# Kernel tuning notes

Hardware: AMD Instinct MI355X
Metric: run time of the kernel (lower is better)

Reference implementation:

```python
import jax, jax.numpy as jnp
import numpy as np

N, E, D = 100000, 1600000, 128
EPS = 1e-5
NUM_LAYERS = 5


def setup_inputs() -> dict:
    key = jax.random.key(0)
    ks = jax.random.split(key, 2 + 2 * NUM_LAYERS)
    inp = {
        "x": jax.random.normal(ks[0], (N, D), dtype=jnp.float32),
        "edge_index": jax.random.randint(ks[1], (2, E), 0, N),
    }
    for i in range(NUM_LAYERS):
        inp[f"W{i}"] = jax.random.normal(ks[2 + 2 * i], (D, D), dtype=jnp.float32) / np.sqrt(D).astype(np.float32)
        inp[f"b{i}"] = jax.random.normal(ks[3 + 2 * i], (D,), dtype=jnp.float32) * 0.01
    return inp


def _gcn_forward(x, edge_index, Ws, bs):
    src, dst = edge_index[0], edge_index[1]
    # Degree with self-loops (torch code appends arange(N) loops, then clamps
    # count at min=1; with loops deg >= 1 always, so clamp is a no-op).
    deg = jax.ops.segment_sum(jnp.ones((E,), x.dtype), dst, num_segments=N) + 1.0
    inv_deg = (1.0 / deg)[:, None]  # [N, 1]
    for W, b in zip(Ws, bs):
        h = x @ W.T  # [N, D] linear (no bias; bias added after aggregation)
        # mean aggregation over in-neighbors + self-loop message (= h itself)
        agg = (jax.ops.segment_sum(h[src], dst, num_segments=N) + h) * inv_deg + b
        # batch_norm in training mode, no affine, biased variance, eps=1e-5
        mean = agg.mean(axis=0)
        var = ((agg - mean) ** 2).mean(axis=0)
        x = jax.nn.relu((agg - mean) * jax.lax.rsqrt(var + EPS))
        # dropout p=0.0, eval mode -> identity
    return x


def reference(x, edge_index, W0, b0, W1, b1, W2, b2, W3, b3, W4, b4):
    return _gcn_forward(x, edge_index, (W0, W1, W2, W3, W4), (b0, b1, b2, b3, b4))
```

## Files before the change

### kernel.cpp

```cpp
#include <hip/hip_runtime.h>
#include <hip/hip_bf16.h>

#define DD 128
#define NPART 8

typedef __bf16 bf16x8 __attribute__((ext_vector_type(8)));
typedef float f32x4 __attribute__((ext_vector_type(4)));

__device__ inline unsigned short f2bf_rne(float f) {
    unsigned u = __float_as_uint(f);
    u += 0x7fff + ((u >> 16) & 1);
    return (unsigned short)(u >> 16);
}


__global__ __launch_bounds__(256) void hist_kernel(const int* __restrict__ dst,
                                                   int* __restrict__ cnt, int E, int psize) {
    int part = blockIdx.x & (NPART - 1);
    int lo = part * psize, hi = lo + psize;
    int stride = (gridDim.x >> 3) * 256;
    for (int e = (blockIdx.x >> 3) * 256 + threadIdx.x; e < E; e += stride) {
        int d = dst[e];
        if (d >= lo && d < hi) atomicAdd(&cnt[d], 1);
    }
}

__global__ void scanA_kernel(const int* __restrict__ cnt, int* __restrict__ row_off,
                             int* __restrict__ partials, int N) {
    __shared__ int ls[256];
    int tid = threadIdx.x;
    int i = blockIdx.x * 1024 + tid * 4;
    int c0 = (i + 0 < N) ? cnt[i + 0] : 0;
    int c1 = (i + 1 < N) ? cnt[i + 1] : 0;
    int c2 = (i + 2 < N) ? cnt[i + 2] : 0;
    int c3 = (i + 3 < N) ? cnt[i + 3] : 0;
    int tot = c0 + c1 + c2 + c3;
    ls[tid] = tot;
    __syncthreads();
    for (int off = 1; off < 256; off <<= 1) {
        int v = (tid >= off) ? ls[tid - off] : 0;
        __syncthreads();
        ls[tid] += v;
        __syncthreads();
    }
    int excl = ls[tid] - tot;
    if (tid == 255) partials[blockIdx.x] = ls[255];
    int e0 = excl, e1 = e0 + c0, e2 = e1 + c1, e3 = e2 + c2;
    if (i + 0 < N) row_off[i + 0] = e0;
    if (i + 1 < N) row_off[i + 1] = e1;
    if (i + 2 < N) row_off[i + 2] = e2;
    if (i + 3 < N) row_off[i + 3] = e3;
}

__global__ __launch_bounds__(256) void scanB_kernel(int* partials, int nb) {
    __shared__ int ls[256];
    int tid = threadIdx.x;
    int base = 0;
    for (int c = 0; c < nb; c += 256) {
        int v = (c + tid < nb) ? partials[c + tid] : 0;
        ls[tid] = v;
        __syncthreads();
        for (int off = 1; off < 256; off <<= 1) {
            int t = (tid >= off) ? ls[tid - off] : 0;
            __syncthreads();
            ls[tid] += t;
            __syncthreads();
        }
        if (c + tid < nb) partials[c + tid] = ls[tid] - v + base;
        int tot = ls[255];
        __syncthreads();
        base += tot;
    }
}

__global__ void scanC_kernel(const int* __restrict__ cnt, int* __restrict__ row_off,
                             int* __restrict__ cursor, float* __restrict__ inv_deg,
                             const int* __restrict__ partials, int N) {
    int tid = threadIdx.x;
    int i = blockIdx.x * 1024 + tid * 4;
    int add = partials[blockIdx.x];
#pragma unroll
    for (int m = 0; m < 4; m++) {
        int idx = i + m;
        if (idx < N) {
            int v = row_off[idx] + add;
            row_off[idx] = v;
            cursor[idx] = v;
            int c = cnt[idx];
            inv_deg[idx] = 1.0f / (float)(c + 1);
            if (idx == N - 1) row_off[N] = v + c;
        }
    }
}

__global__ __launch_bounds__(256) void scatter_kernel(const int* __restrict__ src,
                                                      const int* __restrict__ dst,
                                                      int* __restrict__ cursor,
                                                      int* __restrict__ csr, int E, int psize) {
    int part = blockIdx.x & (NPART - 1);
    int lo = part * psize, hi = lo + psize;
    int stride = (gridDim.x >> 3) * 256;
    for (int e = (blockIdx.x >> 3) * 256 + threadIdx.x; e < E; e += stride) {
        int d = dst[e];
        if (d >= lo && d < hi) {
            int pos = atomicAdd(&cursor[d], 1);
            csr[pos] = src[e];
        }
    }
}


__global__ __launch_bounds__(256) void tobf16_kernel(const float* __restrict__ x,
                                                     unsigned short* __restrict__ h, long total4) {
    long idx = (long)blockIdx.x * 256 + threadIdx.x;
    if (idx >= total4) return;
    float4 v = ((const float4*)x)[idx];
    ushort4 o;
    o.x = f2bf_rne(v.x); o.y = f2bf_rne(v.y); o.z = f2bf_rne(v.z); o.w = f2bf_rne(v.w);
    ((ushort4*)h)[idx] = o;
}


template <int NORM>
__global__ __launch_bounds__(256) void gather_kernel(const unsigned int* __restrict__ prev,
                                                     const int* __restrict__ row_off,
                                                     const int* __restrict__ csr,
                                                     const float* __restrict__ stats_raw,
                                                     float invN,
                                                     unsigned int* __restrict__ outp, int N) {
    int node = blockIdx.x * 4 + (threadIdx.x >> 6);
    if (node >= N) return;
    int lane = threadIdx.x & 63;
    float m0 = 0.f, m1 = 0.f, r0 = 1.f, r1 = 1.f;
    if (NORM) {
        int c = 2 * lane;
        float s0 = stats_raw[c], s1 = stats_raw[c + 1];
        float q0 = stats_raw[128 + c], q1 = stats_raw[129 + c];
        m0 = s0 * invN; m1 = s1 * invN;
        r0 = rsqrtf(q0 * invN - m0 * m0 + 1e-5f);
        r1 = rsqrtf(q1 * invN - m1 * m1 + 1e-5f);
    }
    int base = node * 64 + lane;
    float ax, ay;
    {
        unsigned u = prev[base];
        float vx = __uint_as_float(u << 16);
        float vy = __uint_as_float(u & 0xffff0000u);
        if (NORM) { ax = fmaxf((vx - m0) * r0, 0.f); ay = fmaxf((vy - m1) * r1, 0.f); }
        else      { ax = vx; ay = vy; }
    }
    int e = row_off[node], end = row_off[node + 1];
    for (; e + 8 <= end; e += 8) {
        int i0 = csr[e], i1 = csr[e + 1], i2 = csr[e + 2], i3 = csr[e + 3];
        int i4 = csr[e + 4], i5 = csr[e + 5], i6 = csr[e + 6], i7 = csr[e + 7];
        unsigned u0 = prev[i0 * 64 + lane];
        unsigned u1 = prev[i1 * 64 + lane];
        unsigned u2 = prev[i2 * 64 + lane];
        unsigned u3 = prev[i3 * 64 + lane];
        unsigned u4 = prev[i4 * 64 + lane];
        unsigned u5 = prev[i5 * 64 + lane];
        unsigned u6 = prev[i6 * 64 + lane];
        unsigned u7 = prev[i7 * 64 + lane];
#define GX(u) __uint_as_float((u) << 16)
#define GY(u) __uint_as_float((u) & 0xffff0000u)
        if (NORM) {
            ax += fmaxf((GX(u0) - m0) * r0, 0.f) + fmaxf((GX(u1) - m0) * r0, 0.f)
                + fmaxf((GX(u2) - m0) * r0, 0.f) + fmaxf((GX(u3) - m0) * r0, 0.f)
                + fmaxf((GX(u4) - m0) * r0, 0.f) + fmaxf((GX(u5) - m0) * r0, 0.f)
                + fmaxf((GX(u6) - m0) * r0, 0.f) + fmaxf((GX(u7) - m0) * r0, 0.f);
            ay += fmaxf((GY(u0) - m1) * r1, 0.f) + fmaxf((GY(u1) - m1) * r1, 0.f)
                + fmaxf((GY(u2) - m1) * r1, 0.f) + fmaxf((GY(u3) - m1) * r1, 0.f)
                + fmaxf((GY(u4) - m1) * r1, 0.f) + fmaxf((GY(u5) - m1) * r1, 0.f)
                + fmaxf((GY(u6) - m1) * r1, 0.f) + fmaxf((GY(u7) - m1) * r1, 0.f);
        } else {
            ax += GX(u0) + GX(u1) + GX(u2) + GX(u3) + GX(u4) + GX(u5) + GX(u6) + GX(u7);
            ay += GY(u0) + GY(u1) + GY(u2) + GY(u3) + GY(u4) + GY(u5) + GY(u6) + GY(u7);
        }
    }
    for (; e < end; e++) {
        unsigned u0 = prev[csr[e] * 64 + lane];
        if (NORM) { ax += fmaxf((GX(u0) - m0) * r0, 0.f); ay += fmaxf((GY(u0) - m1) * r1, 0.f); }
        else      { ax += GX(u0); ay += GY(u0); }
    }
#undef GX
#undef GY
    outp[base] = ((unsigned)f2bf_rne(ay) << 16) | (unsigned)f2bf_rne(ax);
}


__global__ void wsplit_kernel(const float* __restrict__ W0, const float* __restrict__ W1,
                              const float* __restrict__ W2, const float* __restrict__ W3,
                              const float* __restrict__ W4, unsigned short* __restrict__ whl) {
    int idx = blockIdx.x * 256 + threadIdx.x;
    int l = idx >> 14, r = idx & 16383;
    const float* W = (l == 0) ? W0 : (l == 1) ? W1 : (l == 2) ? W2 : (l == 3) ? W3 : W4;
    float x = W[r];
    unsigned u = __float_as_uint(x);
    unsigned short h = (unsigned short)(u >> 16);
    float hf = __uint_as_float(u & 0xffff0000u);
    float lo = x - hf;
    unsigned short lw = (unsigned short)(__float_as_uint(lo) >> 16);
    whl[l * 32768 + r] = h;
    whl[l * 32768 + 16384 + r] = lw;
}


__global__ __launch_bounds__(256) void mgemm_kernel(const unsigned short* __restrict__ Sh,
                                                    unsigned short* __restrict__ hb,
                                                    const unsigned short* __restrict__ Whl,
                                                    const float* __restrict__ bias,
                                                    const float* __restrict__ inv_deg,
                                                    float* __restrict__ stats, int N) {
    __shared__ unsigned short ShL[128 * 128];
    const int t = threadIdx.x;
    const int i0 = blockIdx.x * 128;

#pragma unroll
    for (int b = 0; b < 8; b++) {
        int f = b * 256 + t;
        int r = f >> 4, k8 = f & 15;
        int row = i0 + r;
        uint4 v = make_uint4(0u, 0u, 0u, 0u);
        if (row < N) v = *(const uint4*)&Sh[(size_t)row * 128 + k8 * 8];
        *(uint4*)(ShL + r * 128 + ((k8 ^ (r & 7)) * 8)) = v;
    }
    __syncthreads();

    const int w = t >> 6, l = t & 63;
    const int ll = l & 15, lh = l >> 4;
    const unsigned short* Wh = Whl;
    const unsigned short* Wl2 = Whl + 16384;
    f32x4 acc[2][8];
#pragma unroll
    for (int st = 0; st < 2; st++)
#pragma unroll
        for (int jt = 0; jt < 8; jt++) acc[st][jt] = (f32x4){0.f, 0.f, 0.f, 0.f};

    const int r0 = w * 32 + ll;
    const int r1 = r0 + 16;
#pragma unroll
    for (int ks = 0; ks < 4; ks++) {
        int k8 = ks * 4 + lh;
        bf16x8 ah0 = *(const bf16x8*)(ShL + r0 * 128 + ((k8 ^ (r0 & 7)) * 8));
        bf16x8 ah1 = *(const bf16x8*)(ShL + r1 * 128 + ((k8 ^ (r1 & 7)) * 8));
        int wk = ks * 32 + lh * 8;
#pragma unroll
        for (int jt = 0; jt < 8; jt++) {
            int wrow = jt * 16 + ll;
            bf16x8 bh = *(const bf16x8*)(Wh + wrow * 128 + wk);
            bf16x8 bl = *(const bf16x8*)(Wl2 + wrow * 128 + wk);
            acc[0][jt] = __builtin_amdgcn_mfma_f32_16x16x32_bf16(ah0, bh, acc[0][jt], 0, 0, 0);
            acc[1][jt] = __builtin_amdgcn_mfma_f32_16x16x32_bf16(ah1, bh, acc[1][jt], 0, 0, 0);
            acc[0][jt] = __builtin_amdgcn_mfma_f32_16x16x32_bf16(ah0, bl, acc[0][jt], 0, 0, 0);
            acc[1][jt] = __builtin_amdgcn_mfma_f32_16x16x32_bf16(ah1, bl, acc[1][jt], 0, 0, 0);
        }
    }

    float bj[8];
#pragma unroll
    for (int jt = 0; jt < 8; jt++) bj[jt] = bias[jt * 16 + ll];
    float cs[8], cq[8];
#pragma unroll
    for (int jt = 0; jt < 8; jt++) { cs[jt] = 0.f; cq[jt] = 0.f; }
#pragma unroll
    for (int st = 0; st < 2; st++) {
#pragma unroll
        for (int reg = 0; reg < 4; reg++) {
            int row = i0 + w * 32 + st * 16 + lh * 4 + reg;
            bool valid = row < N;
            float sc = valid ? inv_deg[row] : 0.f;
#pragma unroll
            for (int jt = 0; jt < 8; jt++) {
                float o = acc[st][jt][reg] * sc + bj[jt];
                if (valid) {
                    hb[(size_t)row * 128 + jt * 16 + ll] = f2bf_rne(o);
                    cs[jt] += o;
                    cq[jt] += o * o;
                }
            }
        }
    }
#pragma unroll
    for (int jt = 0; jt < 8; jt++) {
        cs[jt] += __shfl_xor(cs[jt], 16);
        cs[jt] += __shfl_xor(cs[jt], 32);
        cq[jt] += __shfl_xor(cq[jt], 16);
        cq[jt] += __shfl_xor(cq[jt], 32);
    }
    __syncthreads();
    float* sred = (float*)ShL;
    if (l < 16) {
#pragma unroll
        for (int jt = 0; jt < 8; jt++) {
            sred[w * 256 + jt * 16 + l] = cs[jt];
            sred[w * 256 + 128 + jt * 16 + l] = cq[jt];
        }
    }
    __syncthreads();
    {
        int col = t & 127, s = t >> 7;
        float v = sred[0 * 256 + s * 128 + col] + sred[1 * 256 + s * 128 + col]
                + sred[2 * 256 + s * 128 + col] + sred[3 * 256 + s * 128 + col];
        atomicAdd(&stats[s * 128 + col], v);
    }
}


__global__ __launch_bounds__(256) void outnorm_kernel(const unsigned int* __restrict__ hb,
                                                      const float* __restrict__ stats_raw,
                                                      float invN,
                                                      float2* __restrict__ out, int total) {
    __shared__ float mls[128], rls[128];
    int t = threadIdx.x;
    if (t < 128) {
        float mean = stats_raw[t] * invN;
        float var = stats_raw[128 + t] * invN - mean * mean;
        mls[t] = mean;
        rls[t] = rsqrtf(var + 1e-5f);
    }
    __syncthreads();
    int stride = gridDim.x * 256;
    for (int idx = blockIdx.x * 256 + t; idx < total; idx += stride) {
        int c = (idx & 63) * 2;
        unsigned u = hb[idx];
        float x = __uint_as_float(u << 16);
        float y = __uint_as_float(u & 0xffff0000u);
        float2 o;
        o.x = fmaxf((x - mls[c]) * rls[c], 0.f);
        o.y = fmaxf((y - mls[c + 1]) * rls[c + 1], 0.f);
        out[idx] = o;
    }
}


extern "C" void kernel_launch(void* const* d_in, const int* in_sizes, int n_in,
                              void* d_out, int out_size, void* d_ws, size_t ws_size,
                              hipStream_t stream) {
    const float* x = (const float*)d_in[0];
    const int* ei = (const int*)d_in[1];
    int N = in_sizes[0] / DD;
    int E = in_sizes[1] / 2;
    const float* Wp[5];
    const float* bp[5];
    for (int l = 0; l < 5; l++) {
        Wp[l] = (const float*)d_in[2 + 2 * l];
        bp[l] = (const float*)d_in[3 + 2 * l];
    }

    char* ws = (char*)d_ws;
    size_t off = 0;
    auto alloc = [&](size_t bytes) -> char* {
        char* p = ws + off;
        off = (off + bytes + 511) & ~(size_t)511;
        return p;
    };
    int* cnt = (int*)alloc((size_t)N * 4);
    int* row_off = (int*)alloc(((size_t)N + 1) * 4);
    int* cursor = (int*)alloc((size_t)N * 4);
    int* partials = (int*)alloc(4096 * 4);
    float* inv_deg = (float*)alloc((size_t)N * 4);
    float* stats = (float*)alloc(5 * 256 * 4);
    unsigned short* whl = (unsigned short*)alloc(5 * 32768 * 2);
    int* csr = (int*)alloc((size_t)E * 4);
    unsigned short* hb = (unsigned short*)alloc((size_t)N * DD * 2);
    unsigned short* Sh = (unsigned short*)alloc((size_t)N * DD * 2);
    (void)ws_size;

    const int* srcv = ei;
    const int* dstv = ei + E;

    hipMemsetAsync(cnt, 0, (size_t)N * 4, stream);
    hipMemsetAsync(stats, 0, 5 * 256 * 4, stream);

    wsplit_kernel<<<5 * 16384 / 256, 256, 0, stream>>>(Wp[0], Wp[1], Wp[2], Wp[3], Wp[4], whl);

    long total4 = (long)N * (DD / 4);
    tobf16_kernel<<<(int)((total4 + 255) / 256), 256, 0, stream>>>(x, hb, total4);

    int psize = (N + NPART - 1) / NPART;
    hist_kernel<<<NPART * 256, 256, 0, stream>>>(dstv, cnt, E, psize);
    int nb = (N + 1023) / 1024;
    scanA_kernel<<<nb, 256, 0, stream>>>(cnt, row_off, partials, N);
    scanB_kernel<<<1, 256, 0, stream>>>(partials, nb);
    scanC_kernel<<<nb, 256, 0, stream>>>(cnt, row_off, cursor, inv_deg, partials, N);
    scatter_kernel<<<NPART * 256, 256, 0, stream>>>(srcv, dstv, cursor, csr, E, psize);

    float invN = 1.0f / (float)N;
    int gblocks = (N + 3) / 4;
    int mblocks = (N + 127) / 128;

    for (int l = 0; l < 5; l++) {
        if (l == 0) {
            gather_kernel<0><<<gblocks, 256, 0, stream>>>((const unsigned int*)hb, row_off, csr,
                                                          nullptr, invN, (unsigned int*)Sh, N);
        } else {
            gather_kernel<1><<<gblocks, 256, 0, stream>>>((const unsigned int*)hb, row_off, csr,
                                                          stats + (l - 1) * 256, invN,
                                                          (unsigned int*)Sh, N);
        }
        mgemm_kernel<<<mblocks, 256, 0, stream>>>(Sh, hb, whl + l * 32768, bp[l], inv_deg,
                                                  stats + l * 256, N);
    }

    int totalU = N * 64;
    outnorm_kernel<<<2048, 256, 0, stream>>>((const unsigned int*)hb, stats + 4 * 256, invN,
                                             (float2*)d_out, totalU);
}
```

Before: 1.007 ms.

## Vectorize gather with 16-byte row loads, stage W in LDS, split normalization

The gather kernel now has each lane load 16-byte chunks, so a wavefront processes four neighbor rows per step and combines the partial sums with cross-lane shuffles. The BatchNorm+ReLU that used to be applied to every gathered neighbor is moved into a separate per-layer norm kernel that writes a normalized bf16 buffer. This removes redundant per-edge normalization work but adds an extra full pass over node features each layer. The GEMM now stages the high and low W halves into swizzled shared memory instead of reading them from global memory per tile, and the output kernel is widened to 8 elements per thread.

```diff
diff --git a/kernel.cpp b/kernel.cpp
--- a/kernel.cpp
+++ b/kernel.cpp
@@ -121,70 +121,67 @@
 }
 
 
-template <int NORM>
-__global__ __launch_bounds__(256) void gather_kernel(const unsigned int* __restrict__ prev,
+#define ACC8(u)                                                         \
+    do {                                                                \
+        a[0] += __uint_as_float((u).x << 16);                           \
+        a[1] += __uint_as_float((u).x & 0xffff0000u);                   \
+        a[2] += __uint_as_float((u).y << 16);                           \
+        a[3] += __uint_as_float((u).y & 0xffff0000u);                   \
+        a[4] += __uint_as_float((u).z << 16);                           \
+        a[5] += __uint_as_float((u).z & 0xffff0000u);                   \
+        a[6] += __uint_as_float((u).w << 16);                           \
+        a[7] += __uint_as_float((u).w & 0xffff0000u);                   \
+    } while (0)
+
+__global__ __launch_bounds__(256) void gather_kernel(const uint4* __restrict__ prev4,
                                                      const int* __restrict__ row_off,
                                                      const int* __restrict__ csr,
-                                                     const float* __restrict__ stats_raw,
-                                                     float invN,
-                                                     unsigned int* __restrict__ outp, int N) {
+                                                     uint4* __restrict__ out4, int N) {
     int node = blockIdx.x * 4 + (threadIdx.x >> 6);
     if (node >= N) return;
     int lane = threadIdx.x & 63;
-    float m0 = 0.f, m1 = 0.f, r0 = 1.f, r1 = 1.f;
-    if (NORM) {
-        int c = 2 * lane;
-        float s0 = stats_raw[c], s1 = stats_raw[c + 1];
-        float q0 = stats_raw[128 + c], q1 = stats_raw[129 + c];
-        m0 = s0 * invN; m1 = s1 * invN;
-        r0 = rsqrtf(q0 * invN - m0 * m0 + 1e-5f);
-        r1 = rsqrtf(q1 * invN - m1 * m1 + 1e-5f);
-    }
-    int base = node * 64 + lane;
-    float ax, ay;
-    {
-        unsigned u = prev[base];
-        float vx = __uint_as_float(u << 16);
-        float vy = __uint_as_float(u & 0xffff0000u);
-        if (NORM) { ax = fmaxf((vx - m0) * r0, 0.f); ay = fmaxf((vy - m1) * r1, 0.f); }
-        else      { ax = vx; ay = vy; }
-    }
+    int g = lane >> 4, c = lane & 15;
+    float a[8];
+#pragma unroll
+    for (int j = 0; j < 8; j++) a[j] = 0.f;
     int e = row_off[node], end = row_off[node + 1];
     for (; e + 8 <= end; e += 8) {
-        int i0 = csr[e], i1 = csr[e + 1], i2 = csr[e + 2], i3 = csr[e + 3];
-        int i4 = csr[e + 4], i5 = csr[e + 5], i6 = csr[e + 6], i7 = csr[e + 7];
-        unsigned u0 = prev[i0 * 64 + lane];
-        unsigned u1 = prev[i1 * 64 + lane];
-        unsigned u2 = prev[i2 * 64 + lane];
-        unsigned u3 = prev[i3 * 64 + lane];
-        unsigned u4 = prev[i4 * 64 + lane];
-        unsigned u5 = prev[i5 * 64 + lane];
-        unsigned u6 = prev[i6 * 64 + lane];
-        unsigned u7 = prev[i7 * 64 + lane];
-#define GX(u) __uint_as_float((u) << 16)
-#define GY(u) __uint_as_float((u) & 0xffff0000u)
-        if (NORM) {
-            ax += fmaxf((GX(u0) - m0) * r0, 0.f) + fmaxf((GX(u1) - m0) * r0, 0.f)
-                + fmaxf((GX(u2) - m0) * r0, 0.f) + fmaxf((GX(u3) - m0) * r0, 0.f)
-                + fmaxf((GX(u4) - m0) * r0, 0.f) + fmaxf((GX(u5) - m0) * r0, 0.f)
-                + fmaxf((GX(u6) - m0) * r0, 0.f) + fmaxf((GX(u7) - m0) * r0, 0.f);
-            ay += fmaxf((GY(u0) - m1) * r1, 0.f) + fmaxf((GY(u1) - m1) * r1, 0.f)
-                + fmaxf((GY(u2) - m1) * r1, 0.f) + fmaxf((GY(u3) - m1) * r1, 0.f)
-                + fmaxf((GY(u4) - m1) * r1, 0.f) + fmaxf((GY(u5) - m1) * r1, 0.f)
-                + fmaxf((GY(u6) - m1) * r1, 0.f) + fmaxf((GY(u7) - m1) * r1, 0.f);
-        } else {
-            ax += GX(u0) + GX(u1) + GX(u2) + GX(u3) + GX(u4) + GX(u5) + GX(u6) + GX(u7);
-            ay += GY(u0) + GY(u1) + GY(u2) + GY(u3) + GY(u4) + GY(u5) + GY(u6) + GY(u7);
-        }
-    }
-    for (; e < end; e++) {
-        unsigned u0 = prev[csr[e] * 64 + lane];
-        if (NORM) { ax += fmaxf((GX(u0) - m0) * r0, 0.f); ay += fmaxf((GY(u0) - m1) * r1, 0.f); }
-        else      { ax += GX(u0); ay += GY(u0); }
-    }
-#undef GX
-#undef GY
-    outp[base] = ((unsigned)f2bf_rne(ay) << 16) | (unsigned)f2bf_rne(ax);
+        int ia = csr[e + g];
+        int ib = csr[e + 4 + g];
+        uint4 ua = prev4[ia * 16 + c];
+        uint4 ub = prev4[ib * 16 + c];
+        ACC8(ua);
+        ACC8(ub);
+    }
+    if (e + 4 <= end) {
+        int ia = csr[e + g];
+        uint4 ua = prev4[ia * 16 + c];
+        ACC8(ua);
+        e += 4;
+    }
+    {
+        int rem = end - e;
+        if (g < rem) {
+            int ia = csr[e + g];
+            uint4 ua = prev4[ia * 16 + c];
+            ACC8(ua);
+        }
+    }
+#pragma unroll
+    for (int j = 0; j < 8; j++) {
+        a[j] += __shfl_xor(a[j], 16);
+        a[j] += __shfl_xor(a[j], 32);
+    }
+    if (g == 0) {
+        uint4 us = prev4[node * 16 + c];
+        ACC8(us);
+        uint4 o;
+        o.x = ((unsigned)f2bf_rne(a[1]) << 16) | f2bf_rne(a[0]);
+        o.y = ((unsigned)f2bf_rne(a[3]) << 16) | f2bf_rne(a[2]);
+        o.z = ((unsigned)f2bf_rne(a[5]) << 16) | f2bf_rne(a[4]);
+        o.w = ((unsigned)f2bf_rne(a[7]) << 16) | f2bf_rne(a[6]);
+        out4[node * 16 + c] = o;
+    }
 }
 
 
@@ -205,13 +202,14 @@
 }
 
 
-__global__ __launch_bounds__(256) void mgemm_kernel(const unsigned short* __restrict__ Sh,
+__global__ __launch_bounds__(256) void mgemm_kernel(const unsigned short* __restrict__ Sg,
                                                     unsigned short* __restrict__ hb,
                                                     const unsigned short* __restrict__ Whl,
                                                     const float* __restrict__ bias,
                                                     const float* __restrict__ inv_deg,
                                                     float* __restrict__ stats, int N) {
-    __shared__ unsigned short ShL[128 * 128];
+    __shared__ unsigned short SL[128 * 128];
+    __shared__ unsigned short WL[128 * 128];
     const int t = threadIdx.x;
     const int i0 = blockIdx.x * 128;
 
@@ -221,38 +219,61 @@
         int r = f >> 4, k8 = f & 15;
         int row = i0 + r;
         uint4 v = make_uint4(0u, 0u, 0u, 0u);
-        if (row < N) v = *(const uint4*)&Sh[(size_t)row * 128 + k8 * 8];
-        *(uint4*)(ShL + r * 128 + ((k8 ^ (r & 7)) * 8)) = v;
+        if (row < N) v = *(const uint4*)&Sg[(size_t)row * 128 + k8 * 8];
+        int lbase = r * 128 + ((k8 ^ (r & 7)) * 8);
+        *(uint4*)(SL + lbase) = v;
+        uint4 wv = *(const uint4*)&Whl[f * 8];
+        *(uint4*)(WL + lbase) = wv;
     }
     __syncthreads();
 
     const int w = t >> 6, l = t & 63;
     const int ll = l & 15, lh = l >> 4;
-    const unsigned short* Wh = Whl;
-    const unsigned short* Wl2 = Whl + 16384;
-    f32x4 acc[2][8];
-#pragma unroll
-    for (int st = 0; st < 2; st++)
-#pragma unroll
-        for (int jt = 0; jt < 8; jt++) acc[st][jt] = (f32x4){0.f, 0.f, 0.f, 0.f};
-
-    const int r0 = w * 32 + ll;
-    const int r1 = r0 + 16;
+    const int r0 = w * 32 + ll, r1 = r0 + 16;
+
+    bf16x8 a0[4], a1[4];
 #pragma unroll
     for (int ks = 0; ks < 4; ks++) {
         int k8 = ks * 4 + lh;
-        bf16x8 ah0 = *(const bf16x8*)(ShL + r0 * 128 + ((k8 ^ (r0 & 7)) * 8));
-        bf16x8 ah1 = *(const bf16x8*)(ShL + r1 * 128 + ((k8 ^ (r1 & 7)) * 8));
-        int wk = ks * 32 + lh * 8;
+        a0[ks] = *(const bf16x8*)(SL + r0 * 128 + ((k8 ^ (r0 & 7)) * 8));
+        a1[ks] = *(const bf16x8*)(SL + r1 * 128 + ((k8 ^ (r1 & 7)) * 8));
+    }
+
+    f32x4 acc[2][8];
+#pragma unroll
+    for (int st = 0; st < 2; st++)
+#pragma unroll
+        for (int jt = 0; jt < 8; jt++) acc[st][jt] = (f32x4){0.f, 0.f, 0.f, 0.f};
+
+#pragma unroll
+    for (int ks = 0; ks < 4; ks++) {
+        int k8 = ks * 4 + lh;
 #pragma unroll
         for (int jt = 0; jt < 8; jt++) {
             int wrow = jt * 16 + ll;
-            bf16x8 bh = *(const bf16x8*)(Wh + wrow * 128 + wk);
-            bf16x8 bl = *(const bf16x8*)(Wl2 + wrow * 128 + wk);
-            acc[0][jt] = __builtin_amdgcn_mfma_f32_16x16x32_bf16(ah0, bh, acc[0][jt], 0, 0, 0);
-            acc[1][jt] = __builtin_amdgcn_mfma_f32_16x16x32_bf16(ah1, bh, acc[1][jt], 0, 0, 0);
-            acc[0][jt] = __builtin_amdgcn_mfma_f32_16x16x32_bf16(ah0, bl, acc[0][jt], 0, 0, 0);
-            acc[1][jt] = __builtin_amdgcn_mfma_f32_16x16x32_bf16(ah1, bl, acc[1][jt], 0, 0, 0);
+            bf16x8 bh = *(const bf16x8*)(WL + wrow * 128 + ((k8 ^ (wrow & 7)) * 8));
+            acc[0][jt] = __builtin_amdgcn_mfma_f32_16x16x32_bf16(a0[ks], bh, acc[0][jt], 0, 0, 0);
+            acc[1][jt] = __builtin_amdgcn_mfma_f32_16x16x32_bf16(a1[ks], bh, acc[1][jt], 0, 0, 0);
+        }
+    }
+    __syncthreads();
+#pragma unroll
+    for (int b = 0; b < 8; b++) {
+        int f = b * 256 + t;
+        int r = f >> 4, k8 = f & 15;
+        uint4 wv = *(const uint4*)&Whl[16384 + f * 8];
+        *(uint4*)(WL + r * 128 + ((k8 ^ (r & 7)) * 8)) = wv;
+    }
+    __syncthreads();
+#pragma unroll
+    for (int ks = 0; ks < 4; ks++) {
+        int k8 = ks * 4 + lh;
+#pragma unroll
+        for (int jt = 0; jt < 8; jt++) {
+            int wrow = jt * 16 + ll;
+            bf16x8 bl = *(const bf16x8*)(WL + wrow * 128 + ((k8 ^ (wrow & 7)) * 8));
+            acc[0][jt] = __builtin_amdgcn_mfma_f32_16x16x32_bf16(a0[ks], bl, acc[0][jt], 0, 0, 0);
+            acc[1][jt] = __builtin_amdgcn_mfma_f32_16x16x32_bf16(a1[ks], bl, acc[1][jt], 0, 0, 0);
         }
     }
 
@@ -288,7 +309,7 @@
         cq[jt] += __shfl_xor(cq[jt], 32);
     }
     __syncthreads();
-    float* sred = (float*)ShL;
+    float* sred = (float*)SL;
     if (l < 16) {
 #pragma unroll
         for (int jt = 0; jt < 8; jt++) {
@@ -306,10 +327,10 @@
 }
 
 
-__global__ __launch_bounds__(256) void outnorm_kernel(const unsigned int* __restrict__ hb,
-                                                      const float* __restrict__ stats_raw,
-                                                      float invN,
-                                                      float2* __restrict__ out, int total) {
+__global__ __launch_bounds__(256) void norm_kernel(const uint4* __restrict__ hb4,
+                                                   const float* __restrict__ stats_raw,
+                                                   float invN,
+                                                   uint4* __restrict__ hn4, int totalQ) {
     __shared__ float mls[128], rls[128];
     int t = threadIdx.x;
     if (t < 128) {
@@ -320,15 +341,55 @@
     }
     __syncthreads();
     int stride = gridDim.x * 256;
-    for (int idx = blockIdx.x * 256 + t; idx < total; idx += stride) {
-        int c = (idx & 63) * 2;
-        unsigned u = hb[idx];
-        float x = __uint_as_float(u << 16);
-        float y = __uint_as_float(u & 0xffff0000u);
-        float2 o;
-        o.x = fmaxf((x - mls[c]) * rls[c], 0.f);
-        o.y = fmaxf((y - mls[c + 1]) * rls[c + 1], 0.f);
-        out[idx] = o;
+    for (int idx = blockIdx.x * 256 + t; idx < totalQ; idx += stride) {
+        int c0 = (idx & 15) * 8;
+        uint4 u = hb4[idx];
+        float v[8];
+        v[0] = __uint_as_float(u.x << 16); v[1] = __uint_as_float(u.x & 0xffff0000u);
+        v[2] = __uint_as_float(u.y << 16); v[3] = __uint_as_float(u.y & 0xffff0000u);
+        v[4] = __uint_as_float(u.z << 16); v[5] = __uint_as_float(u.z & 0xffff0000u);
+        v[6] = __uint_as_float(u.w << 16); v[7] = __uint_as_float(u.w & 0xffff0000u);
+#pragma unroll
+        for (int j = 0; j < 8; j++) v[j] = fmaxf((v[j] - mls[c0 + j]) * rls[c0 + j], 0.f);
+        uint4 o;
+        o.x = ((unsigned)f2bf_rne(v[1]) << 16) | f2bf_rne(v[0]);
+        o.y = ((unsigned)f2bf_rne(v[3]) << 16) | f2bf_rne(v[2]);
+        o.z = ((unsigned)f2bf_rne(v[5]) << 16) | f2bf_rne(v[4]);
+        o.w = ((unsigned)f2bf_rne(v[7]) << 16) | f2bf_rne(v[6]);
+        hn4[idx] = o;
+    }
+}
+
+
+__global__ __launch_bounds__(256) void outnorm_kernel(const uint4* __restrict__ hb4,
+                                                      const float* __restrict__ stats_raw,
+                                                      float invN,
+                                                      float4* __restrict__ out4, int totalQ) {
+    __shared__ float mls[128], rls[128];
+    int t = threadIdx.x;
+    if (t < 128) {
+        float mean = stats_raw[t] * invN;
+        float var = stats_raw[128 + t] * invN - mean * mean;
+        mls[t] = mean;
+        rls[t] = rsqrtf(var + 1e-5f);
+    }
+    __syncthreads();
+    int stride = gridDim.x * 256;
+    for (int idx = blockIdx.x * 256 + t; idx < totalQ; idx += stride) {
+        int c0 = (idx & 15) * 8;
+        uint4 u = hb4[idx];
+        float v[8];
+        v[0] = __uint_as_float(u.x << 16); v[1] = __uint_as_float(u.x & 0xffff0000u);
+        v[2] = __uint_as_float(u.y << 16); v[3] = __uint_as_float(u.y & 0xffff0000u);
+        v[4] = __uint_as_float(u.z << 16); v[5] = __uint_as_float(u.z & 0xffff0000u);
+        v[6] = __uint_as_float(u.w << 16); v[7] = __uint_as_float(u.w & 0xffff0000u);
+#pragma unroll
+        for (int j = 0; j < 8; j++) v[j] = fmaxf((v[j] - mls[c0 + j]) * rls[c0 + j], 0.f);
+        float4 o0, o1;
+        o0.x = v[0]; o0.y = v[1]; o0.z = v[2]; o0.w = v[3];
+        o1.x = v[4]; o1.y = v[5]; o1.z = v[6]; o1.w = v[7];
+        out4[idx * 2 + 0] = o0;
+        out4[idx * 2 + 1] = o1;
     }
 }
 
@@ -362,8 +423,9 @@
     float* stats = (float*)alloc(5 * 256 * 4);
     unsigned short* whl = (unsigned short*)alloc(5 * 32768 * 2);
     int* csr = (int*)alloc((size_t)E * 4);
+    unsigned short* hn = (unsigned short*)alloc((size_t)N * DD * 2);
+    unsigned short* Sg = (unsigned short*)alloc((size_t)N * DD * 2);
     unsigned short* hb = (unsigned short*)alloc((size_t)N * DD * 2);
-    unsigned short* Sh = (unsigned short*)alloc((size_t)N * DD * 2);
     (void)ws_size;
 
     const int* srcv = ei;
@@ -375,7 +437,7 @@
     wsplit_kernel<<<5 * 16384 / 256, 256, 0, stream>>>(Wp[0], Wp[1], Wp[2], Wp[3], Wp[4], whl);
 
     long total4 = (long)N * (DD / 4);
-    tobf16_kernel<<<(int)((total4 + 255) / 256), 256, 0, stream>>>(x, hb, total4);
+    tobf16_kernel<<<(int)((total4 + 255) / 256), 256, 0, stream>>>(x, hn, total4);
 
     int psize = (N + NPART - 1) / NPART;
     hist_kernel<<<NPART * 256, 256, 0, stream>>>(dstv, cnt, E, psize);
@@ -388,21 +450,19 @@
     float invN = 1.0f / (float)N;
     int gblocks = (N + 3) / 4;
     int mblocks = (N + 127) / 128;
+    int totalQ = N * 16;
 
     for (int l = 0; l < 5; l++) {
-        if (l == 0) {
-            gather_kernel<0><<<gblocks, 256, 0, stream>>>((const unsigned int*)hb, row_off, csr,
-                                                          nullptr, invN, (unsigned int*)Sh, N);
-        } else {
-            gather_kernel<1><<<gblocks, 256, 0, stream>>>((const unsigned int*)hb, row_off, csr,
-                                                          stats + (l - 1) * 256, invN,
-                                                          (unsigned int*)Sh, N);
-        }
-        mgemm_kernel<<<mblocks, 256, 0, stream>>>(Sh, hb, whl + l * 32768, bp[l], inv_deg,
+        gather_kernel<<<gblocks, 256, 0, stream>>>((const uint4*)hn, row_off, csr,
+                                                   (uint4*)Sg, N);
+        mgemm_kernel<<<mblocks, 256, 0, stream>>>(Sg, hb, whl + l * 32768, bp[l], inv_deg,
                                                   stats + l * 256, N);
-    }
-
-    int totalU = N * 64;
-    outnorm_kernel<<<2048, 256, 0, stream>>>((const unsigned int*)hb, stats + 4 * 256, invN,
-                                             (float2*)d_out, totalU);
-}
+        if (l < 4) {
+            norm_kernel<<<2048, 256, 0, stream>>>((const uint4*)hb, stats + l * 256, invN,
+                                                  (uint4*)hn, totalQ);
+        }
+    }
+
+    outnorm_kernel<<<2048, 256, 0, stream>>>((const uint4*)hb, stats + 4 * 256, invN,
+                                             (float4*)d_out, totalQ);
+}
```

Result: faster. 846.0 us (-16.0%).
